# Performance work log

Hardware: AMD Instinct MI355X
Metric: run time of the kernel (lower is better)

Reference implementation:

```python
import jax, jax.numpy as jnp
import numpy as np

B, S, NT, D, NU = 1024, 200, 10000, 256, 100000
BETA_1 = 0.1


def setup_inputs() -> dict:
    key = jax.random.key(0)
    ks = jax.random.split(key, 6)
    user_id = jax.random.randint(ks[0], (B,), 0, NU)
    event_type = jax.random.randint(ks[1], (B, S), 0, NT + 1)  # 0 = pad
    adjacent_matrix = jax.random.uniform(ks[2], (NT, NT), dtype=jnp.float32)
    pop_encoding = jax.random.normal(ks[3], (NT + 1, D), dtype=jnp.float32)
    event_emb = jax.random.normal(ks[4], (NT + 1, D), dtype=jnp.float32) * 0.02
    user_emb = jax.random.normal(ks[5], (NU, D), dtype=jnp.float32) * 0.02
    return dict(user_id=user_id, event_type=event_type,
                adjacent_matrix=adjacent_matrix, pop_encoding=pop_encoding,
                evaluation=0, event_emb=event_emb, user_emb=user_emb)


def _l2norm(x, eps):
    # tf.nn.l2_normalize: x * rsqrt(max(sum(x^2), eps))
    return x * jax.lax.rsqrt(jnp.maximum(jnp.sum(x * x, axis=-1, keepdims=True), eps))


def reference(user_id, event_type, adjacent_matrix, pop_encoding, evaluation, event_emb, user_emb):
    non_pad = (event_type != 0).astype(jnp.float32)[..., None]          # [B,S,1]
    enc = event_emb[event_type]                                          # [B,S,D]
    usr = user_emb[user_id]                                              # [B,D]
    pop = pop_encoding[event_type] * non_pad                             # [B,S,D]
    # enc += sign(enc) * l2_normalize(user_output) (default eps 1e-12)
    enc = enc + jnp.sign(enc) * _l2norm(usr, 1e-12)[:, None, :]
    # per-sample adjacency: two-axis gather of the item-item matrix
    idx = jnp.where(event_type > 0, event_type - 1, 0)                   # [B,S]
    adj = adjacent_matrix[idx[:, :, None], idx[:, None, :]]              # [B,S,S]
    has_valid = (jnp.sum(event_type > 0, axis=1) > 0).astype(jnp.float32)
    adj = adj * has_valid[:, None, None]  # rows with all-pad stay zero, as in the loop
    output = jnp.mean(enc, axis=1)                                       # [B,D]
    user_embeddings = jnp.concatenate([output, jnp.mean(pop, axis=1) * BETA_1], axis=-1)  # [B,2D]
    if evaluation:
        item_encoding = event_emb[1:]                                    # [NT,D]
        scores = user_embeddings[:, :D] @ item_encoding.T
    else:
        item_encoding = jnp.concatenate([event_emb[1:], pop_encoding[1:] * BETA_1], axis=-1)  # [NT,2D]
        scores = user_embeddings @ item_encoding.T                       # [B,NT]
    prediction = jnp.tanh(_l2norm(scores, 1e-05))
    return prediction, user_embeddings, pop, adj
```

## Files before the change

kernel.cpp:

```cpp
#include <hip/hip_runtime.h>
#include <math.h>

#define NB 1024
#define NS 200
#define NTOK 10000
#define ND 256
#define BETA 0.1f

static constexpr size_t PRED_OFF = 0;
static constexpr size_t UE_OFF   = (size_t)NB * NTOK;
static constexpr size_t POP_OFF  = UE_OFF + (size_t)NB * 2 * ND;
static constexpr size_t ADJ_OFF  = POP_OFF + (size_t)NB * NS * ND;

static constexpr size_t WS_SIDX   = 0;
static constexpr size_t WS_HV     = WS_SIDX + (size_t)NB * NS;
static constexpr size_t WS_COUNTS = WS_HV + NB;
static constexpr size_t WS_OFFS   = WS_COUNTS + NTOK;
static constexpr size_t WS_CURSOR = WS_OFFS + NTOK + 1;
static constexpr size_t WS_PAIRS  = WS_CURSOR + NTOK;
static constexpr size_t WS_UEBF   = 440640;
static constexpr size_t WS_IEBF   = WS_UEBF + 262144;

typedef __attribute__((ext_vector_type(8))) short bf16x8;
typedef __attribute__((ext_vector_type(4))) float f32x4;
typedef __attribute__((ext_vector_type(8))) unsigned short u16x8;

static __device__ inline unsigned short f2bf(float f) {
    unsigned int u = __float_as_uint(f);
    return (unsigned short)((u + 0x7fffu + ((u >> 16) & 1u)) >> 16);
}

__global__ __launch_bounds__(256) void k_front(
    const int* __restrict__ user_id,
    const int* __restrict__ event_type,
    const float* __restrict__ pop_encoding,
    const float* __restrict__ event_emb,
    const float* __restrict__ user_emb,
    float* __restrict__ ue,
    unsigned short* __restrict__ ue_bf,
    float* __restrict__ pop,
    int* __restrict__ sidx_all,
    float* __restrict__ hvf,
    int* __restrict__ counts,
    unsigned short* __restrict__ ie)
{
    const int t = threadIdx.x;

    if (blockIdx.x >= NB) {
        const int idx = (blockIdx.x - NB) * 256 + t;
        const int row = idx >> 7;
        const int kq  = idx & 127;
        float4 v; float sc;
        if (kq < 64) { v = *(const float4*)&event_emb[(size_t)(row + 1) * ND + kq * 4]; sc = 1.f; }
        else         { v = *(const float4*)&pop_encoding[(size_t)(row + 1) * ND + (kq - 64) * 4]; sc = BETA; }
        ushort4 h = {f2bf(v.x * sc), f2bf(v.y * sc), f2bf(v.z * sc), f2bf(v.w * sc)};
        *(ushort4*)&ie[(size_t)row * 512 + kq * 4] = h;
        return;
    }

    const int b  = blockIdx.x;
    const int sg = t >> 6;
    const int tl = t & 63;

    const int uid = user_id[b];
    const float4 u4 = *(const float4*)&user_emb[(size_t)uid * ND + tl * 4];

    float ss = u4.x * u4.x + u4.y * u4.y + u4.z * u4.z + u4.w * u4.w;
    #pragma unroll
    for (int o = 32; o > 0; o >>= 1) ss += __shfl_xor(ss, o, 64);
    const float rn = rsqrtf(fmaxf(ss, 1e-12f));
    const float4 nu4 = {u4.x * rn, u4.y * rn, u4.z * rn, u4.w * rn};

    __shared__ int et_s[NS];
    __shared__ int hv_s;
    if (t == 0) hv_s = 0;
    if (t < NS) et_s[t] = event_type[(size_t)b * NS + t];
    __syncthreads();

    if (t < NS) {
        const int et = et_s[t];
        const int r  = (et > 0) ? (et - 1) : 0;
        sidx_all[(size_t)b * NS + t] = r;
        atomicAdd(&counts[r], 1);
        if (et > 0) hv_s = 1;
    }

    float4 eacc = {0.f, 0.f, 0.f, 0.f};
    float4 pacc = {0.f, 0.f, 0.f, 0.f};
    #pragma unroll 2
    for (int it = 0; it < NS / 4; ++it) {
        const int s  = sg + 4 * it;
        const int et = et_s[s];
        const float4 e = *(const float4*)&event_emb[(size_t)et * ND + tl * 4];
        float4 p = *(const float4*)&pop_encoding[(size_t)et * ND + tl * 4];
        const float z = (et != 0) ? 1.f : 0.f;
        p.x *= z; p.y *= z; p.z *= z; p.w *= z;
        eacc.x += e.x + ((e.x > 0.f) ? nu4.x : ((e.x < 0.f) ? -nu4.x : 0.f));
        eacc.y += e.y + ((e.y > 0.f) ? nu4.y : ((e.y < 0.f) ? -nu4.y : 0.f));
        eacc.z += e.z + ((e.z > 0.f) ? nu4.z : ((e.z < 0.f) ? -nu4.z : 0.f));
        eacc.w += e.w + ((e.w > 0.f) ? nu4.w : ((e.w < 0.f) ? -nu4.w : 0.f));
        pacc.x += p.x; pacc.y += p.y; pacc.z += p.z; pacc.w += p.w;
        const f32x4 pv = {p.x, p.y, p.z, p.w};
        __builtin_nontemporal_store(pv, (f32x4*)&pop[((size_t)b * NS + s) * ND + tl * 4]);
    }

    __shared__ __align__(16) float4 es[4][64];
    __shared__ __align__(16) float4 ps[4][64];
    es[sg][tl] = eacc;
    ps[sg][tl] = pacc;
    __syncthreads();

    if (t < 128) {
        const int half = t >> 6;
        const int l2   = t & 63;
        float4 f = half ? ps[0][l2] : es[0][l2];
        #pragma unroll
        for (int w = 1; w < 4; ++w) {
            const float4 g = half ? ps[w][l2] : es[w][l2];
            f.x += g.x; f.y += g.y; f.z += g.z; f.w += g.w;
        }
        const float sc = half ? (BETA / NS) : (1.f / NS);
        const float4 o = {f.x * sc, f.y * sc, f.z * sc, f.w * sc};
        const size_t off = (size_t)b * 512 + half * 256 + l2 * 4;
        *(float4*)&ue[off] = o;
        ushort4 h = {f2bf(o.x), f2bf(o.y), f2bf(o.z), f2bf(o.w)};
        *(ushort4*)&ue_bf[off] = h;
    }
    if (t == 0) hvf[b] = hv_s ? 1.f : 0.f;
}

#define SCAN_CHUNK 40
__global__ __launch_bounds__(256) void k_scan(
    const int* __restrict__ counts,
    int* __restrict__ offsets,
    int* __restrict__ cursor)
{
    const int t = threadIdx.x;
    int sum = 0;
    int local[SCAN_CHUNK];
    #pragma unroll
    for (int k = 0; k < SCAN_CHUNK; ++k) {
        const int idx = t * SCAN_CHUNK + k;
        const int c = (idx < NTOK) ? counts[idx] : 0;
        local[k] = c;
        sum += c;
    }
    __shared__ int part[256];
    part[t] = sum;
    __syncthreads();
    for (int o = 1; o < 256; o <<= 1) {
        const int v = (t >= o) ? part[t - o] : 0;
        __syncthreads();
        part[t] += v;
        __syncthreads();
    }
    int running = part[t] - sum;
    #pragma unroll
    for (int k = 0; k < SCAN_CHUNK; ++k) {
        const int idx = t * SCAN_CHUNK + k;
        if (idx < NTOK) {
            offsets[idx] = running;
            cursor[idx]  = running;
            running += local[k];
        }
    }
    if (t == 255) offsets[NTOK] = part[255];
}

__global__ __launch_bounds__(256) void k_scatter(
    const int* __restrict__ sidx_all,
    int* __restrict__ cursor,
    int* __restrict__ pairs)
{
    const int b = blockIdx.x;
    const int t = threadIdx.x;
    if (t < NS) {
        const int r = sidx_all[(size_t)b * NS + t];
        const int slot = atomicAdd(&cursor[r], 1);
        pairs[slot] = b * NS + t;
    }
}

__global__ __launch_bounds__(512) void k_adj2(
    const float* __restrict__ A,
    const int* __restrict__ sidx_all,
    const int* __restrict__ offsets,
    const int* __restrict__ pairs,
    const float* __restrict__ hvf,
    float* __restrict__ adj)
{
    const int r = blockIdx.x;
    const int t = threadIdx.x;
    const int p0 = offsets[r];
    const int n  = offsets[r + 1] - p0;
    if (n == 0) return;

    __shared__ __align__(16) float rowlds[NTOK];
    const float4* Arow = (const float4*)(A + (size_t)r * NTOK);
    #pragma unroll 5
    for (int l = t; l < NTOK / 4; l += 512)
        ((float4*)rowlds)[l] = Arow[l];
    __syncthreads();

    const int wave = t >> 6, lane = t & 63;
    #pragma unroll 2
    for (int pi = wave; pi < n; pi += 8) {
        const int pv = pairs[p0 + pi];
        const int b  = pv / NS;
        const float hv = hvf[b];
        if (lane < 50) {
            const int4 c4 = *(const int4*)&sidx_all[(size_t)b * NS + lane * 4];
            f32x4 v;
            v.x = rowlds[c4.x] * hv;
            v.y = rowlds[c4.y] * hv;
            v.z = rowlds[c4.z] * hv;
            v.w = rowlds[c4.w] * hv;
            __builtin_nontemporal_store(v, (f32x4*)&adj[(size_t)pv * NS + lane * 4]);
        }
    }
}

#define GBM 128
#define GBN 128
#define GBK 32
#define LDK 40

__global__ __launch_bounds__(256) void k_gemm_mfma(
    const unsigned short* __restrict__ ue_bf,
    const unsigned short* __restrict__ ie_bf,
    float* __restrict__ scores)
{
    __shared__ __align__(16) unsigned short As[GBM * LDK];
    __shared__ __align__(16) unsigned short Bs[GBN * LDK];

    const int t  = threadIdx.x;
    const int bn = blockIdx.x, bm = blockIdx.y;
    const int m0 = bm * GBM, n0 = bn * GBN;

    const int wave = t >> 6, lane = t & 63;
    const int ww = wave & 1, wm = wave >> 1;
    const int lr = lane & 15;
    const int kg = lane >> 4;

    f32x4 acc[4][4] = {};

    for (int k0 = 0; k0 < 512; k0 += GBK) {
        #pragma unroll
        for (int i = 0; i < 2; ++i) {
            const int c = t + 256 * i;
            const int row = c >> 2, q = c & 3;
            *(u16x8*)&As[row * LDK + q * 8] =
                *(const u16x8*)&ue_bf[(size_t)(m0 + row) * 512 + k0 + q * 8];
        }
        #pragma unroll
        for (int i = 0; i < 2; ++i) {
            const int c = t + 256 * i;
            const int row = c >> 2, q = c & 3;
            const int gn = n0 + row;
            u16x8 h = {0, 0, 0, 0, 0, 0, 0, 0};
            if (gn < NTOK)
                h = *(const u16x8*)&ie_bf[(size_t)gn * 512 + k0 + q * 8];
            *(u16x8*)&Bs[row * LDK + q * 8] = h;
        }
        __syncthreads();

        bf16x8 a[4], b[4];
        #pragma unroll
        for (int mf = 0; mf < 4; ++mf)
            a[mf] = *(const bf16x8*)&As[(wm * 64 + mf * 16 + lr) * LDK + kg * 8];
        #pragma unroll
        for (int nf = 0; nf < 4; ++nf)
            b[nf] = *(const bf16x8*)&Bs[(ww * 64 + nf * 16 + lr) * LDK + kg * 8];
        #pragma unroll
        for (int mf = 0; mf < 4; ++mf)
            #pragma unroll
            for (int nf = 0; nf < 4; ++nf)
                acc[mf][nf] = __builtin_amdgcn_mfma_f32_16x16x32_bf16(
                    a[mf], b[nf], acc[mf][nf], 0, 0, 0);
        __syncthreads();
    }

    #pragma unroll
    for (int mf = 0; mf < 4; ++mf) {
        const int row = m0 + wm * 64 + mf * 16 + kg * 4;
        #pragma unroll
        for (int nf = 0; nf < 4; ++nf) {
            const int col = n0 + ww * 64 + nf * 16 + lr;
            if (col < NTOK) {
                #pragma unroll
                for (int r = 0; r < 4; ++r)
                    scores[(size_t)(row + r) * NTOK + col] = acc[mf][nf][r];
            }
        }
    }
}

__global__ __launch_bounds__(256) void k_norm(float* __restrict__ scores)
{
    const int b = blockIdx.x;
    const int t = threadIdx.x;
    float4* row4 = (float4*)(scores + (size_t)b * NTOK);

    float ss = 0.f;
    for (int l = t; l < NTOK / 4; l += 256) {
        const float4 v = row4[l];
        ss += v.x * v.x + v.y * v.y + v.z * v.z + v.w * v.w;
    }
    #pragma unroll
    for (int o = 32; o > 0; o >>= 1) ss += __shfl_down(ss, o, 64);
    __shared__ float wss[4];
    const int wid = t >> 6, lane = t & 63;
    if (lane == 0) wss[wid] = ss;
    __syncthreads();
    const float tot = wss[0] + wss[1] + wss[2] + wss[3];
    const float rs = rsqrtf(fmaxf(tot, 1e-5f));

    for (int l = t; l < NTOK / 4; l += 256) {
        float4 v = row4[l];
        v.x = tanhf(v.x * rs); v.y = tanhf(v.y * rs);
        v.z = tanhf(v.z * rs); v.w = tanhf(v.w * rs);
        row4[l] = v;
    }
}

extern "C" void kernel_launch(void* const* d_in, const int* in_sizes, int n_in,
                              void* d_out, int out_size, void* d_ws, size_t ws_size,
                              hipStream_t stream) {
    const int*   user_id      = (const int*)d_in[0];
    const int*   event_type   = (const int*)d_in[1];
    const float* adjacent     = (const float*)d_in[2];
    const float* pop_encoding = (const float*)d_in[3];
    const float* event_emb    = (const float*)d_in[5];
    const float* user_emb     = (const float*)d_in[6];

    float* out  = (float*)d_out;
    float* pred = out + PRED_OFF;
    float* ue   = out + UE_OFF;
    float* pop  = out + POP_OFF;
    float* adj  = out + ADJ_OFF;

    int*   ws       = (int*)d_ws;
    int*   sidx_all = ws + WS_SIDX;
    float* hvf      = (float*)(ws + WS_HV);
    int*   counts   = ws + WS_COUNTS;
    int*   offsets  = ws + WS_OFFS;
    int*   cursor   = ws + WS_CURSOR;
    int*   pairs    = ws + WS_PAIRS;
    unsigned short* ue_bf = (unsigned short*)(ws + WS_UEBF);
    unsigned short* ie_bf = (unsigned short*)(ws + WS_IEBF);

    hipMemsetAsync(counts, 0, NTOK * sizeof(int), stream);
    k_front<<<NB + 5000, 256, 0, stream>>>(user_id, event_type, pop_encoding,
                                           event_emb, user_emb, ue, ue_bf, pop,
                                           sidx_all, hvf, counts, ie_bf);
    k_scan<<<1, 256, 0, stream>>>(counts, offsets, cursor);
    k_scatter<<<NB, 256, 0, stream>>>(sidx_all, cursor, pairs);
    k_adj2<<<NTOK, 512, 0, stream>>>(adjacent, sidx_all, offsets, pairs, hvf, adj);
    dim3 ggrid((NTOK + GBN - 1) / GBN, NB / GBM);
    k_gemm_mfma<<<ggrid, 256, 0, stream>>>(ue_bf, ie_bf, pred);
    k_norm<<<NB, 256, 0, stream>>>(pred);
}
```

Before: 315.6 us.

## Fuse adjacency gather and scores GEMM into one interleaved launch

Merges the adjacency-row gather kernel and the bf16 MFMA scores GEMM into a single kernel. Every 16th block, for the first 632 groups, runs a GEMM tile and the remaining blocks do adjacency rows. The aim is to overlap the compute-bound GEMM with the memory-bound gather and save one launch. In exchange, the adjacency blocks drop from 512 to 256 threads and share a 40KB shared-memory buffer, which can lower per-block bandwidth and occupancy.

```diff
diff --git a/kernel.cpp b/kernel.cpp
--- a/kernel.cpp
+++ b/kernel.cpp
@@ -181,7 +181,16 @@
     }
 }
 
-__global__ __launch_bounds__(512) void k_adj2(
+#define GBM 128
+#define GBN 128
+#define GBK 32
+#define LDK 40
+#define NGEMM 632
+
+__global__ __launch_bounds__(256) void k_main(
+    const unsigned short* __restrict__ ue_bf,
+    const unsigned short* __restrict__ ie_bf,
+    float* __restrict__ scores,
     const float* __restrict__ A,
     const int* __restrict__ sidx_all,
     const int* __restrict__ offsets,
@@ -189,22 +198,91 @@
     const float* __restrict__ hvf,
     float* __restrict__ adj)
 {
-    const int r = blockIdx.x;
-    const int t = threadIdx.x;
+    __shared__ __align__(16) unsigned char smem[40960];
+    const int bid = blockIdx.x;
+    const int t   = threadIdx.x;
+
+    const int g = bid >> 4;
+    if ((bid & 15) == 0 && g < NGEMM) {
+        unsigned short* As = (unsigned short*)smem;
+        unsigned short* Bs = As + GBM * LDK;
+
+        const int bn = g % 79, bm = g / 79;
+        const int m0 = bm * GBM, n0 = bn * GBN;
+
+        const int wave = t >> 6, lane = t & 63;
+        const int ww = wave & 1, wm = wave >> 1;
+        const int lr = lane & 15;
+        const int kg = lane >> 4;
+
+        f32x4 acc[4][4] = {};
+
+        for (int k0 = 0; k0 < 512; k0 += GBK) {
+            #pragma unroll
+            for (int i = 0; i < 2; ++i) {
+                const int c = t + 256 * i;
+                const int row = c >> 2, q = c & 3;
+                *(u16x8*)&As[row * LDK + q * 8] =
+                    *(const u16x8*)&ue_bf[(size_t)(m0 + row) * 512 + k0 + q * 8];
+            }
+            #pragma unroll
+            for (int i = 0; i < 2; ++i) {
+                const int c = t + 256 * i;
+                const int row = c >> 2, q = c & 3;
+                const int gn = n0 + row;
+                u16x8 h = {0, 0, 0, 0, 0, 0, 0, 0};
+                if (gn < NTOK)
+                    h = *(const u16x8*)&ie_bf[(size_t)gn * 512 + k0 + q * 8];
+                *(u16x8*)&Bs[row * LDK + q * 8] = h;
+            }
+            __syncthreads();
+
+            bf16x8 a[4], b[4];
+            #pragma unroll
+            for (int mf = 0; mf < 4; ++mf)
+                a[mf] = *(const bf16x8*)&As[(wm * 64 + mf * 16 + lr) * LDK + kg * 8];
+            #pragma unroll
+            for (int nf = 0; nf < 4; ++nf)
+                b[nf] = *(const bf16x8*)&Bs[(ww * 64 + nf * 16 + lr) * LDK + kg * 8];
+            #pragma unroll
+            for (int mf = 0; mf < 4; ++mf)
+                #pragma unroll
+                for (int nf = 0; nf < 4; ++nf)
+                    acc[mf][nf] = __builtin_amdgcn_mfma_f32_16x16x32_bf16(
+                        a[mf], b[nf], acc[mf][nf], 0, 0, 0);
+            __syncthreads();
+        }
+
+        #pragma unroll
+        for (int mf = 0; mf < 4; ++mf) {
+            const int row = m0 + wm * 64 + mf * 16 + kg * 4;
+            #pragma unroll
+            for (int nf = 0; nf < 4; ++nf) {
+                const int col = n0 + ww * 64 + nf * 16 + lr;
+                if (col < NTOK) {
+                    #pragma unroll
+                    for (int r = 0; r < 4; ++r)
+                        scores[(size_t)(row + r) * NTOK + col] = acc[mf][nf][r];
+                }
+            }
+        }
+        return;
+    }
+
+    const int r = bid - min(g + 1, NGEMM);
     const int p0 = offsets[r];
     const int n  = offsets[r + 1] - p0;
     if (n == 0) return;
 
-    __shared__ __align__(16) float rowlds[NTOK];
+    float* rowlds = (float*)smem;
     const float4* Arow = (const float4*)(A + (size_t)r * NTOK);
-    #pragma unroll 5
-    for (int l = t; l < NTOK / 4; l += 512)
+    #pragma unroll 4
+    for (int l = t; l < NTOK / 4; l += 256)
         ((float4*)rowlds)[l] = Arow[l];
     __syncthreads();
 
     const int wave = t >> 6, lane = t & 63;
-    #pragma unroll 2
-    for (int pi = wave; pi < n; pi += 8) {
+    for (int pi = wave; pi < n; pi += 4) {
         const int pv = pairs[p0 + pi];
         const int b  = pv / NS;
         const float hv = hvf[b];
@@ -220,81 +298,6 @@
     }
 }
 
-#define GBM 128
-#define GBN 128
-#define GBK 32
-#define LDK 40
-
-__global__ __launch_bounds__(256) void k_gemm_mfma(
-    const unsigned short* __restrict__ ue_bf,
-    const unsigned short* __restrict__ ie_bf,
-    float* __restrict__ scores)
-{
-    __shared__ __align__(16) unsigned short As[GBM * LDK];
-    __shared__ __align__(16) unsigned short Bs[GBN * LDK];
-
-    const int t  = threadIdx.x;
-    const int bn = blockIdx.x, bm = blockIdx.y;
-    const int m0 = bm * GBM, n0 = bn * GBN;
-
-    const int wave = t >> 6, lane = t & 63;
-    const int ww = wave & 1, wm = wave >> 1;
-    const int lr = lane & 15;
-    const int kg = lane >> 4;
-
-    f32x4 acc[4][4] = {};
-
-    for (int k0 = 0; k0 < 512; k0 += GBK) {
-        #pragma unroll
-        for (int i = 0; i < 2; ++i) {
-            const int c = t + 256 * i;
-            const int row = c >> 2, q = c & 3;
-            *(u16x8*)&As[row * LDK + q * 8] =
-                *(const u16x8*)&ue_bf[(size_t)(m0 + row) * 512 + k0 + q * 8];
-        }
-        #pragma unroll
-        for (int i = 0; i < 2; ++i) {
-            const int c = t + 256 * i;
-            const int row = c >> 2, q = c & 3;
-            const int gn = n0 + row;
-            u16x8 h = {0, 0, 0, 0, 0, 0, 0, 0};
-            if (gn < NTOK)
-                h = *(const u16x8*)&ie_bf[(size_t)gn * 512 + k0 + q * 8];
-            *(u16x8*)&Bs[row * LDK + q * 8] = h;
-        }
-        __syncthreads();
-
-        bf16x8 a[4], b[4];
-        #pragma unroll
-        for (int mf = 0; mf < 4; ++mf)
-            a[mf] = *(const bf16x8*)&As[(wm * 64 + mf * 16 + lr) * LDK + kg * 8];
-        #pragma unroll
-        for (int nf = 0; nf < 4; ++nf)
-            b[nf] = *(const bf16x8*)&Bs[(ww * 64 + nf * 16 + lr) * LDK + kg * 8];
-        #pragma unroll
-        for (int mf = 0; mf < 4; ++mf)
-            #pragma unroll
-            for (int nf = 0; nf < 4; ++nf)
-                acc[mf][nf] = __builtin_amdgcn_mfma_f32_16x16x32_bf16(
-                    a[mf], b[nf], acc[mf][nf], 0, 0, 0);
-        __syncthreads();
-    }
-
-    #pragma unroll
-    for (int mf = 0; mf < 4; ++mf) {
-        const int row = m0 + wm * 64 + mf * 16 + kg * 4;
-        #pragma unroll
-        for (int nf = 0; nf < 4; ++nf) {
-            const int col = n0 + ww * 64 + nf * 16 + lr;
-            if (col < NTOK) {
-                #pragma unroll
-                for (int r = 0; r < 4; ++r)
-                    scores[(size_t)(row + r) * NTOK + col] = acc[mf][nf][r];
-            }
-        }
-    }
-}
-
 __global__ __launch_bounds__(256) void k_norm(float* __restrict__ scores)
 {
     const int b = blockIdx.x;
@@ -355,8 +358,8 @@
                                            sidx_all, hvf, counts, ie_bf);
     k_scan<<<1, 256, 0, stream>>>(counts, offsets, cursor);
     k_scatter<<<NB, 256, 0, stream>>>(sidx_all, cursor, pairs);
-    k_adj2<<<NTOK, 512, 0, stream>>>(adjacent, sidx_all, offsets, pairs, hvf, adj);
-    dim3 ggrid((NTOK + GBN - 1) / GBN, NB / GBM);
-    k_gemm_mfma<<<ggrid, 256, 0, stream>>>(ue_bf, ie_bf, pred);
+    k_main<<<NTOK + NGEMM, 256, 0, stream>>>(ue_bf, ie_bf, pred,
+                                             adjacent, sidx_all, offsets, pairs,
+                                             hvf, adj);
     k_norm<<<NB, 256, 0, stream>>>(pred);
 }
```

Measured after the change: 537.4 us. +70.3%, slower.
